# Performance work log

Hardware: AMD Instinct MI355X
Metric: run time of the kernel (lower is better)

The kernel has to match this reference:

```python
import jax, jax.numpy as jnp
import numpy as np

N = 100000      # nodes
E = 1000000     # edges per directional view
D = 128         # feature dim (all layers)
NG, OG = 4, 32  # n_gram_len, one_gram_dim (NG*OG == D)
L = 2           # conv layers (layer_dims=[128,128,128])
DEC = 64        # decoder hidden = D // 2
CLS = 64        # task classes
L2_EPS = 1e-12


def setup_inputs() -> dict:
    key = jax.random.key(0)
    ks = iter(jax.random.split(key, 40))
    nrm = lambda shape, s=0.05: jax.random.normal(next(ks), shape, dtype=jnp.float32) * s
    inp = {
        'x': jax.random.normal(next(ks), (N, D), dtype=jnp.float32),
        'edge_index_in': jax.random.randint(next(ks), (2, E), 0, N, dtype=jnp.int32),
        'edge_weight_in': jax.random.uniform(next(ks), (E,), dtype=jnp.float32),
        'edge_index_out': jax.random.randint(next(ks), (2, E), 0, N, dtype=jnp.int32),
        'edge_weight_out': jax.random.uniform(next(ks), (E,), dtype=jnp.float32),
        'edge_index_und': jax.random.randint(next(ks), (2, E), 0, N, dtype=jnp.int32),
        'edge_weight_und': jax.random.uniform(next(ks), (E,), dtype=jnp.float32),
        'pe': nrm((NG, OG)),
        # per-layer stacked params (both layers are D->D)
        'W_main_in': nrm((L, D, D)),
        'W_main_out': nrm((L, D, D)),
        'W_shared': nrm((L, D, D)),
        'W_und': nrm((L, D, D)),
        'b_main_in': nrm((L, D), 0.01),
        'b_main_out': nrm((L, D), 0.01),
        'b_shared_in': nrm((L, D), 0.01),
        'b_shared_out': nrm((L, D), 0.01),
        'b_und': nrm((L, D), 0.01),
        'C_in_vec': jnp.ones((L, N, 1), jnp.float32) + nrm((L, N, 1), 0.01),
        'C_out_vec': jnp.ones((L, N, 1), jnp.float32) + nrm((L, N, 1), 0.01),
        'C_all_vec': jnp.ones((L, N, 1), jnp.float32) + nrm((L, N, 1), 0.01),
        'constant': nrm((L, N, D)),
        'Wd1': nrm((DEC, D)),
        'bd1': nrm((DEC,), 0.01),
        'Wd2': nrm((CLS, DEC)),
        'bd2': nrm((CLS,), 0.01),
    }
    return inp


def reference(x, edge_index_in, edge_weight_in, edge_index_out, edge_weight_out,
              edge_index_und, edge_weight_und, pe,
              W_main_in, W_main_out, W_shared, W_und,
              b_main_in, b_main_out, b_shared_in, b_shared_out, b_und,
              C_in_vec, C_out_vec, C_all_vec, constant,
              Wd1, bd1, Wd2, bd2):
    n = x.shape[0]

    def prop(ei, ew, h):
        # message: edge_weight * x_j (gather from src=ei[0]); aggr='add' at dst=ei[1]
        msg = ew[:, None] * h[ei[0]]                      # [E, D]
        return jax.ops.segment_sum(msg, ei[1], num_segments=n)

    # positional encoding over n-gram sub-blocks
    h = (x.reshape(n, NG, OG) + pe[None]).reshape(n, NG * OG)

    for i in range(L):
        h_res = h
        hs = h @ W_shared[i].T                            # shared transform (computed once)
        ic = (prop(edge_index_in, edge_weight_in, h @ W_main_in[i].T) + b_main_in[i]
              + prop(edge_index_in, edge_weight_in, hs) + b_shared_in[i])
        oc = (prop(edge_index_out, edge_weight_out, h @ W_main_out[i].T) + b_main_out[i]
              + prop(edge_index_out, edge_weight_out, hs) + b_shared_out[i])
        ac = prop(edge_index_und, edge_weight_und, h @ W_und[i].T) + b_und[i]
        gcn = C_all_vec[i] * ac + C_in_vec[i] * ic + C_out_vec[i] * oc + constant[i]
        # res_proj is Identity (in_dim == out_dim); dropout inactive (eval)
        h = jax.nn.leaky_relu(gcn + h_res)

    z = jax.nn.relu(h @ Wd1.T + bd1)
    logits = z @ Wd2.T + bd2
    logp = jax.nn.log_softmax(logits, axis=-1)
    emb = h / jnp.maximum(jnp.linalg.norm(h, axis=-1, keepdims=True), L2_EPS)
    return (logp, emb)
```

## Files before the change

kernel.cpp:

```cpp
#include <hip/hip_runtime.h>
#include <math.h>

#define NN 100000
#define EE 1000000
#define DD 128
#define CLS 64

#define NB 196
#define CHUNK 4096
#define NCH 245
#define SLOTS (3 * NB * NCH)
#define CAPB 8192

typedef short bf16x8 __attribute__((ext_vector_type(8)));
typedef float f32x4 __attribute__((ext_vector_type(4)));

static __device__ __forceinline__ short f2bf(float f) {
  union { float f; unsigned u; } v; v.f = f;
  unsigned r = v.u + 0x7FFF + ((v.u >> 16) & 1);
  return (short)(r >> 16);
}
static __device__ __forceinline__ unsigned pack2(float a, float b) {
  return ((unsigned)(unsigned short)f2bf(b) << 16) | (unsigned short)f2bf(a);
}
static __device__ __forceinline__ float bf_lo(unsigned u) {
  union { unsigned u; float f; } v; v.u = u << 16; return v.f;
}
static __device__ __forceinline__ float bf_hi(unsigned u) {
  union { unsigned u; float f; } v; v.u = u & 0xffff0000u; return v.f;
}

__global__ __launch_bounds__(256) void pe_kernel(const float* __restrict__ x,
                                                 const float* __restrict__ pe,
                                                 short* __restrict__ h) {
  int idx8 = blockIdx.x * 256 + threadIdx.x;
  int d0 = (idx8 & 15) * 8;
  float4 a = *(const float4*)&x[(size_t)idx8 * 8];
  float4 b = *(const float4*)&x[(size_t)idx8 * 8 + 4];
  float4 pa = *(const float4*)&pe[d0];
  float4 pb = *(const float4*)&pe[d0 + 4];
  int4 o;
  o.x = pack2(a.x + pa.x, a.y + pa.y);
  o.y = pack2(a.z + pa.z, a.w + pa.w);
  o.z = pack2(b.x + pb.x, b.y + pb.y);
  o.w = pack2(b.z + pb.z, b.w + pb.w);
  *(int4*)&h[(size_t)idx8 * 8] = o;
}

__global__ __launch_bounds__(256) void wprep_kernel(const float* __restrict__ Wmi,
                                                    const float* __restrict__ Wmo,
                                                    const float* __restrict__ Wsh,
                                                    const float* __restrict__ Wu,
                                                    short* __restrict__ Wcat) {
  int idx = blockIdx.x * 256 + threadIdx.x;
  int l = idx / 49152;
  int r = idx - l * 49152;
  int j = r >> 7, k = r & 127;
  float v;
  if (j < 128)      v = Wmi[l*16384 + j*128 + k] + Wsh[l*16384 + j*128 + k];
  else if (j < 256) v = Wmo[l*16384 + (j-128)*128 + k] + Wsh[l*16384 + (j-128)*128 + k];
  else              v = Wu[l*16384 + (j-256)*128 + k];
  Wcat[idx] = f2bf(v);
}

__global__ __launch_bounds__(256) void countA_kernel(const int* __restrict__ ei0,
                                                     const int* __restrict__ ei1,
                                                     const int* __restrict__ ei2,
                                                     int* __restrict__ counts) {
  __shared__ int c[NB];
  int v = blockIdx.y, ch = blockIdx.x, tid = threadIdx.x;
  const int* dstp = ((v == 0) ? ei0 : (v == 1) ? ei1 : ei2) + EE;
  for (int i = tid; i < NB; i += 256) c[i] = 0;
  __syncthreads();
  int s = ch * CHUNK, e = (s + CHUNK < EE) ? s + CHUNK : EE;
  for (int i = s + tid; i < e; i += 256) atomicAdd(&c[dstp[i] >> 9], 1);
  __syncthreads();
  for (int b = tid; b < NB; b += 256) counts[(v * NB + b) * NCH + ch] = c[b];
}

__global__ __launch_bounds__(256) void scan1_kernel(const int* __restrict__ counts,
                                                    int* __restrict__ S,
                                                    int* __restrict__ bsums, int n) {
  __shared__ int sd[256];
  int t = threadIdx.x;
  int base = blockIdx.x * 1024 + t * 4;
  int4 v = make_int4(0, 0, 0, 0);
  if (base + 3 < n) {
    v = *(const int4*)&counts[base];
  } else {
    if (base + 0 < n) v.x = counts[base + 0];
    if (base + 1 < n) v.y = counts[base + 1];
    if (base + 2 < n) v.z = counts[base + 2];
    if (base + 3 < n) v.w = counts[base + 3];
  }
  int ts = v.x + v.y + v.z + v.w;
  sd[t] = ts;
  __syncthreads();
  for (int off = 1; off < 256; off <<= 1) {
    int xel = (t >= off) ? sd[t - off] : 0;
    __syncthreads();
    sd[t] += xel;
    __syncthreads();
  }
  int excl = sd[t] - ts;
  int o0 = excl, o1 = o0 + v.x, o2 = o1 + v.y, o3 = o2 + v.z;
  if (base + 0 < n) S[base + 0] = o0;
  if (base + 1 < n) S[base + 1] = o1;
  if (base + 2 < n) S[base + 2] = o2;
  if (base + 3 < n) S[base + 3] = o3;
  if (t == 255) bsums[blockIdx.x] = sd[255];
}

__global__ void scan2_kernel(int* __restrict__ bsums, int nb) {
  __shared__ int sd[512];
  int t = threadIdx.x;
  int v = (t < nb) ? bsums[t] : 0;
  sd[t] = v;
  __syncthreads();
  for (int off = 1; off < 512; off <<= 1) {
    int xel = (t >= off) ? sd[t - off] : 0;
    __syncthreads();
    sd[t] += xel;
    __syncthreads();
  }
  if (t < nb) bsums[t] = sd[t] - v;
}

__global__ __launch_bounds__(256) void scan3_kernel(int* __restrict__ S,
                                                    const int* __restrict__ bsums, int n) {
  int i = blockIdx.x * 256 + threadIdx.x;
  if (i < n) S[i] += bsums[i >> 10];
}

__global__ __launch_bounds__(256) void partA_kernel(const int* __restrict__ ei0,
                                                    const int* __restrict__ ei1,
                                                    const int* __restrict__ ei2,
                                                    const float* __restrict__ ew0,
                                                    const float* __restrict__ ew1,
                                                    const float* __restrict__ ew2,
                                                    const int* __restrict__ S,
                                                    int2* __restrict__ binned) {
  __shared__ int cur[NB];
  int v = blockIdx.y, ch = blockIdx.x, tid = threadIdx.x;
  const int* ei = (v == 0) ? ei0 : (v == 1) ? ei1 : ei2;
  const float* ew = (v == 0) ? ew0 : (v == 1) ? ew1 : ew2;
  for (int b = tid; b < NB; b += 256) cur[b] = S[(v * NB + b) * NCH + ch];
  __syncthreads();
  int s = ch * CHUNK, e = (s + CHUNK < EE) ? s + CHUNK : EE;
  for (int i = s + tid; i < e; i += 256) {
    int src = ei[i];
    int dst = ei[EE + i];
    float w = ew[i];
    int b = dst >> 9;
    int pos = atomicAdd(&cur[b], 1);
    binned[pos] = make_int2(src | ((dst & 511) << 17), __float_as_int(w));
  }
}

__global__ __launch_bounds__(256) void buildB_kernel(const int2* __restrict__ binned,
                                                     const int* __restrict__ S,
                                                     unsigned* __restrict__ csr4,
                                                     int* __restrict__ offs) {
  __shared__ int2 recs[CAPB];
  __shared__ int cnt[512];
  __shared__ int pref[512];
  __shared__ int sd[256];
  int gb = blockIdx.x, tid = threadIdx.x;
  int v = gb / NB, b = gb - v * NB;
  int base = S[gb * NCH];
  int next = (gb == 3 * NB - 1) ? 3 * EE : S[(gb + 1) * NCH];
  int n = next - base;
  for (int i = tid; i < 512; i += 256) cnt[i] = 0;
  int m = n < CAPB ? n : CAPB;
  for (int i = tid; i < m; i += 256) recs[i] = binned[base + i];
  __syncthreads();
  for (int i = tid; i < n; i += 256) {
    int2 r = (i < CAPB) ? recs[i] : binned[base + i];
    atomicAdd(&cnt[(r.x >> 17) & 511], 1);
  }
  __syncthreads();
  int c0 = cnt[2 * tid], c1 = cnt[2 * tid + 1];
  int ssum = c0 + c1;
  sd[tid] = ssum;
  __syncthreads();
  for (int off = 1; off < 256; off <<= 1) {
    int x = (tid >= off) ? sd[tid - off] : 0;
    __syncthreads();
    sd[tid] += x;
    __syncthreads();
  }
  int excl = sd[tid] - ssum;
  pref[2 * tid] = excl;
  pref[2 * tid + 1] = excl + c0;
  __syncthreads();
  int node0 = b * 512;
  for (int i = tid; i < 512; i += 256) {
    int node = node0 + i;
    if (node < NN) offs[v * NN + node] = base + pref[i];
  }
  if (gb == 0 && tid == 0) offs[3 * NN] = 3 * EE;
  for (int i = tid; i < 512; i += 256) cnt[i] = pref[i];
  __syncthreads();
  for (int i = tid; i < n; i += 256) {
    int2 r = (i < CAPB) ? recs[i] : binned[base + i];
    int nl = (r.x >> 17) & 511;
    int p = atomicAdd(&cnt[nl], 1);
    float w = __int_as_float(r.y);
    unsigned wb = (unsigned)(unsigned short)f2bf(w);
    csr4[base + p] = (wb << 17) | (unsigned)(r.x & 0x1FFFF);
  }
}

#define LW 136
__global__ __launch_bounds__(256) void mm_mfma(const short* __restrict__ H,
                                               const short* __restrict__ WcatL,
                                               short* __restrict__ tAll) {
  __shared__ short As[128 * LW];
  __shared__ short Bs[128 * LW];
  int tid = threadIdx.x;
  int rowbase = blockIdx.x * 128;

  for (int idx = tid; idx < 2048; idx += 256) {
    int r = idx >> 4, c8 = (idx & 15) * 8;
    int gr = rowbase + r; if (gr >= NN) gr = NN - 1;
    *(int4*)&As[r * LW + c8] = *(const int4*)&H[(size_t)gr * 128 + c8];
  }

  int w = tid >> 6, lane = tid & 63;
  int wr = (w >> 1) * 64, wc = (w & 1) * 64;
  int lrow = lane & 15, quad = lane >> 4;

  for (int view = 0; view < 3; ++view) {
    __syncthreads();
    for (int idx = tid; idx < 2048; idx += 256) {
      int r = idx >> 4, c8 = (idx & 15) * 8;
      *(int4*)&Bs[r * LW + c8] = *(const int4*)&WcatL[(view * 128 + r) * 128 + c8];
    }
    __syncthreads();

    f32x4 acc[4][4];
#pragma unroll
    for (int mi = 0; mi < 4; ++mi)
#pragma unroll
      for (int ni = 0; ni < 4; ++ni) acc[mi][ni] = (f32x4){0.f, 0.f, 0.f, 0.f};

#pragma unroll
    for (int k0 = 0; k0 < 128; k0 += 32) {
      bf16x8 a[4], b[4];
#pragma unroll
      for (int mi = 0; mi < 4; ++mi)
        a[mi] = *(const bf16x8*)&As[(wr + mi * 16 + lrow) * LW + k0 + quad * 8];
#pragma unroll
      for (int ni = 0; ni < 4; ++ni)
        b[ni] = *(const bf16x8*)&Bs[(wc + ni * 16 + lrow) * LW + k0 + quad * 8];
#pragma unroll
      for (int mi = 0; mi < 4; ++mi)
#pragma unroll
        for (int ni = 0; ni < 4; ++ni)
          acc[mi][ni] = __builtin_amdgcn_mfma_f32_16x16x32_bf16(a[mi], b[ni], acc[mi][ni], 0, 0, 0);
    }

    short* out = tAll + (size_t)view * ((size_t)NN * 128);
#pragma unroll
    for (int mi = 0; mi < 4; ++mi) {
#pragma unroll
      for (int ni = 0; ni < 4; ++ni) {
#pragma unroll
        for (int r = 0; r < 4; ++r) {
          int row = rowbase + wr + mi * 16 + quad * 4 + r;
          if (row < NN) {
            int col = wc + ni * 16 + lrow;
            out[(size_t)row * 128 + col] = f2bf(acc[mi][ni][r]);
          }
        }
      }
    }
  }
}

__global__ __launch_bounds__(256) void agg_kernel(
    const short* __restrict__ tAll, const unsigned* __restrict__ csr4,
    const int* __restrict__ offs, const short* __restrict__ h_prev,
    const float* __restrict__ b_mi, const float* __restrict__ b_mo,
    const float* __restrict__ b_si, const float* __restrict__ b_so,
    const float* __restrict__ b_u, const float* __restrict__ Cin,
    const float* __restrict__ Cout, const float* __restrict__ Call,
    const float* __restrict__ cst, short* __restrict__ h_out) {
  int gid = blockIdx.x * 256 + threadIdx.x;
  int v = gid >> 6;
  int lane = gid & 63;
  int f0 = lane * 2;
  float ax[3], ay[3];

#pragma unroll
  for (int view = 0; view < 3; ++view) {
    const short* t = tAll + (size_t)view * ((size_t)NN * 128);
    int s = offs[view * NN + v];
    int e = offs[view * NN + v + 1];
    float accx = 0.f, accy = 0.f;
    for (int base = s; base < e; base += 64) {
      int cnt = e - base; if (cnt > 64) cnt = 64;
      int r = 0;
      if (lane < cnt) r = (int)csr4[base + lane];
      int j = 0;
      for (; j + 3 < cnt; j += 4) {
        unsigned r0 = (unsigned)__shfl(r, j);
        unsigned r1 = (unsigned)__shfl(r, j + 1);
        unsigned r2 = (unsigned)__shfl(r, j + 2);
        unsigned r3 = (unsigned)__shfl(r, j + 3);
        float w0 = __uint_as_float((r0 >> 17) << 16);
        float w1 = __uint_as_float((r1 >> 17) << 16);
        float w2 = __uint_as_float((r2 >> 17) << 16);
        float w3 = __uint_as_float((r3 >> 17) << 16);
        unsigned u0 = *(const unsigned*)&t[(size_t)(r0 & 0x1FFFF) * 128 + f0];
        unsigned u1 = *(const unsigned*)&t[(size_t)(r1 & 0x1FFFF) * 128 + f0];
        unsigned u2 = *(const unsigned*)&t[(size_t)(r2 & 0x1FFFF) * 128 + f0];
        unsigned u3 = *(const unsigned*)&t[(size_t)(r3 & 0x1FFFF) * 128 + f0];
        accx += w0 * bf_lo(u0) + w1 * bf_lo(u1) + w2 * bf_lo(u2) + w3 * bf_lo(u3);
        accy += w0 * bf_hi(u0) + w1 * bf_hi(u1) + w2 * bf_hi(u2) + w3 * bf_hi(u3);
      }
      for (; j < cnt; ++j) {
        unsigned r0 = (unsigned)__shfl(r, j);
        float w0 = __uint_as_float((r0 >> 17) << 16);
        unsigned u0 = *(const unsigned*)&t[(size_t)(r0 & 0x1FFFF) * 128 + f0];
        accx += w0 * bf_lo(u0);
        accy += w0 * bf_hi(u0);
      }
    }
    ax[view] = accx; ay[view] = accy;
  }

  float ci = Cin[v], co = Cout[v], ca = Call[v];
  float2 bi = *(const float2*)&b_mi[f0];
  float2 bsi2 = *(const float2*)&b_si[f0];
  float2 bo = *(const float2*)&b_mo[f0];
  float2 bso2 = *(const float2*)&b_so[f0];
  float2 bu = *(const float2*)&b_u[f0];
  float2 cs = *(const float2*)&cst[(size_t)v * 128 + f0];
  unsigned hp = *(const unsigned*)&h_prev[(size_t)v * 128 + f0];

  float gx = ca * (ax[2] + bu.x) + ci * (ax[0] + bi.x + bsi2.x) +
             co * (ax[1] + bo.x + bso2.x) + cs.x + bf_lo(hp);
  float gy = ca * (ay[2] + bu.y) + ci * (ay[0] + bi.y + bsi2.y) +
             co * (ay[1] + bo.y + bso2.y) + cs.y + bf_hi(hp);
  gx = gx > 0.f ? gx : 0.01f * gx;
  gy = gy > 0.f ? gy : 0.01f * gy;
  *(unsigned*)&h_out[(size_t)v * 128 + f0] = pack2(gx, gy);
}

__global__ __launch_bounds__(256) void dec_kernel(const short* __restrict__ h,
                                                  const float* __restrict__ Wd1,
                                                  const float* __restrict__ bd1,
                                                  const float* __restrict__ Wd2,
                                                  const float* __restrict__ bd2,
                                                  float* __restrict__ out_logp,
                                                  float* __restrict__ out_emb) {
  __shared__ float Hs[32 * 128];
  __shared__ float W1t[64 * 66];
  __shared__ float W2t[64 * 66];
  __shared__ float Zs[32 * 68];
  int tid = threadIdx.x;
  int base = blockIdx.x * 32;

  for (int idx = tid; idx < 2048; idx += 256) {
    unsigned u = *(const unsigned*)&h[(size_t)base * 128 + idx * 2];
    Hs[idx * 2] = bf_lo(u);
    Hs[idx * 2 + 1] = bf_hi(u);
  }
  for (int idx = tid; idx < 4096; idx += 256) {
    int c = idx >> 6, k = idx & 63;
    W2t[k * 66 + c] = Wd2[idx];
  }

  int j = tid & 63;
  int rg = tid >> 6;
  float zacc[8];
#pragma unroll
  for (int r = 0; r < 8; ++r) zacc[r] = 0.f;

  for (int kk = 0; kk < 128; kk += 64) {
    __syncthreads();
    for (int idx = tid; idx < 4096; idx += 256) {
      int jj = idx >> 6, k = idx & 63;
      W1t[k * 66 + jj] = Wd1[jj * 128 + kk + k];
    }
    __syncthreads();
    for (int k = 0; k < 64; ++k) {
      float w = W1t[k * 66 + j];
#pragma unroll
      for (int r = 0; r < 8; ++r) zacc[r] += Hs[(rg * 8 + r) * 128 + kk + k] * w;
    }
  }
  float b1 = bd1[j];
#pragma unroll
  for (int r = 0; r < 8; ++r) {
    float z = zacc[r] + b1;
    Zs[(rg * 8 + r) * 68 + j] = z > 0.f ? z : 0.f;
  }
  __syncthreads();

  float b2 = bd2[j];
  float lg[8];
#pragma unroll
  for (int i = 0; i < 8; ++i) lg[i] = b2;
  for (int k = 0; k < 64; ++k) {
    float w = W2t[k * 66 + j];
#pragma unroll
    for (int i = 0; i < 8; ++i) lg[i] += Zs[(rg + 4 * i) * 68 + k] * w;
  }

#pragma unroll
  for (int i = 0; i < 8; ++i) {
    float m = lg[i];
    for (int d = 1; d < 64; d <<= 1) m = fmaxf(m, __shfl_xor(m, d));
    float s = expf(lg[i] - m);
    for (int d = 1; d < 64; d <<= 1) s += __shfl_xor(s, d);
    float lp = lg[i] - m - logf(s);
    out_logp[(size_t)(base + rg + 4 * i) * 64 + j] = lp;
  }

#pragma unroll
  for (int i = 0; i < 8; ++i) {
    int r = rg + 4 * i;
    float v1 = Hs[r * 128 + j];
    float v2 = Hs[r * 128 + 64 + j];
    float ss = v1 * v1 + v2 * v2;
    for (int d = 1; d < 64; d <<= 1) ss += __shfl_xor(ss, d);
    float nrm = sqrtf(ss);
    float sc = 1.f / fmaxf(nrm, 1e-12f);
    size_t o = (size_t)(base + r) * 128;
    out_emb[o + j] = v1 * sc;
    out_emb[o + 64 + j] = v2 * sc;
  }
}

extern "C" void kernel_launch(void* const* d_in, const int* in_sizes, int n_in,
                              void* d_out, int out_size, void* d_ws, size_t ws_size,
                              hipStream_t stream) {
  const float* x   = (const float*)d_in[0];
  const int* eiI   = (const int*)d_in[1];
  const float* ewI = (const float*)d_in[2];
  const int* eiO   = (const int*)d_in[3];
  const float* ewO = (const float*)d_in[4];
  const int* eiU   = (const int*)d_in[5];
  const float* ewU = (const float*)d_in[6];
  const float* pe  = (const float*)d_in[7];
  const float* Wmi = (const float*)d_in[8];
  const float* Wmo = (const float*)d_in[9];
  const float* Wsh = (const float*)d_in[10];
  const float* Wu  = (const float*)d_in[11];
  const float* bmi = (const float*)d_in[12];
  const float* bmo = (const float*)d_in[13];
  const float* bsi = (const float*)d_in[14];
  const float* bso = (const float*)d_in[15];
  const float* bu  = (const float*)d_in[16];
  const float* Cin = (const float*)d_in[17];
  const float* Cou = (const float*)d_in[18];
  const float* Cal = (const float*)d_in[19];
  const float* cst = (const float*)d_in[20];
  const float* Wd1 = (const float*)d_in[21];
  const float* bd1 = (const float*)d_in[22];
  const float* Wd2 = (const float*)d_in[23];
  const float* bd2 = (const float*)d_in[24];

  const size_t ND = (size_t)NN * DD;
  short* wsS = (short*)d_ws;
  short* hA   = wsS;
  short* hB   = hA + ND;
  short* tAll = hB + ND;
  short* Wcat = tAll + 3 * ND;
  int2* binned   = (int2*)(Wcat + 98304);
  unsigned* csr4 = (unsigned*)(binned + (size_t)3 * EE);
  int* S      = (int*)(csr4 + (size_t)3 * EE);
  int* bsums  = S + SLOTS + 4;
  int* offs   = bsums + 512;

  pe_kernel<<<6250, 256, 0, stream>>>(x, pe, hA);
  wprep_kernel<<<384, 256, 0, stream>>>(Wmi, Wmo, Wsh, Wu, Wcat);

  dim3 chGrid(NCH, 3);
  countA_kernel<<<chGrid, 256, 0, stream>>>(eiI, eiO, eiU, S);
  const int nb1 = (SLOTS + 1023) / 1024;
  scan1_kernel<<<nb1, 256, 0, stream>>>(S, S, bsums, SLOTS);
  scan2_kernel<<<1, 512, 0, stream>>>(bsums, nb1);
  scan3_kernel<<<(SLOTS + 255) / 256, 256, 0, stream>>>(S, bsums, SLOTS);
  partA_kernel<<<chGrid, 256, 0, stream>>>(eiI, eiO, eiU, ewI, ewO, ewU, S, binned);
  buildB_kernel<<<3 * NB, 256, 0, stream>>>(binned, S, csr4, offs);

  const short* hin = hA;
  short* hout = hB;
  dim3 mmGrid((NN + 127) / 128);
  for (int l = 0; l < 2; ++l) {
    mm_mfma<<<mmGrid, 256, 0, stream>>>(hin, Wcat + l * 49152, tAll);
    agg_kernel<<<25000, 256, 0, stream>>>(tAll, csr4, offs, hin,
                                          bmi + l * DD, bmo + l * DD, bsi + l * DD,
                                          bso + l * DD, bu + l * DD, Cin + l * NN,
                                          Cou + l * NN, Cal + l * NN,
                                          cst + (size_t)l * NN * DD, hout);
    short* tmp = (short*)hin;
    hin = hout;
    hout = tmp;
  }

  float* out_logp = (float*)d_out;
  float* out_emb = out_logp + (size_t)NN * CLS;
  dec_kernel<<<3125, 256, 0, stream>>>(hin, Wd1, bd1, Wd2, bd2, out_logp, out_emb);
}
```

Measured before the change: 790.2 us.

## Stage GEMM output through LDS for vector stores; split aggregation wave into edge halves

The transform GEMM epilogue now writes its bf16 results into shared memory and then stores whole rows to global memory with 16-byte vector writes, instead of scattered 2-byte stores. The aggregation kernel splits each 64-lane wave into two half-waves that each process alternate edges with 8-byte feature loads (4 features per lane). The two halves' partial sums are combined with a cross-lane xor shuffle. This aims to cut store transactions and raise gather width and memory-level parallelism, at the cost of extra syncs, LDS reuse of the B tile, and a final shuffle reduction.

```diff
diff --git a/kernel.cpp b/kernel.cpp
--- a/kernel.cpp
+++ b/kernel.cpp
@@ -260,20 +260,25 @@
           acc[mi][ni] = __builtin_amdgcn_mfma_f32_16x16x32_bf16(a[mi], b[ni], acc[mi][ni], 0, 0, 0);
     }
 
+    __syncthreads();
+#pragma unroll
+    for (int mi = 0; mi < 4; ++mi)
+#pragma unroll
+      for (int ni = 0; ni < 4; ++ni)
+#pragma unroll
+        for (int r = 0; r < 4; ++r) {
+          int rl = wr + mi * 16 + quad * 4 + r;
+          int cl = wc + ni * 16 + lrow;
+          Bs[rl * LW + cl] = f2bf(acc[mi][ni][r]);
+        }
+    __syncthreads();
+
     short* out = tAll + (size_t)view * ((size_t)NN * 128);
-#pragma unroll
-    for (int mi = 0; mi < 4; ++mi) {
-#pragma unroll
-      for (int ni = 0; ni < 4; ++ni) {
-#pragma unroll
-        for (int r = 0; r < 4; ++r) {
-          int row = rowbase + wr + mi * 16 + quad * 4 + r;
-          if (row < NN) {
-            int col = wc + ni * 16 + lrow;
-            out[(size_t)row * 128 + col] = f2bf(acc[mi][ni][r]);
-          }
-        }
-      }
+    for (int idx = tid; idx < 2048; idx += 256) {
+      int r = idx >> 4, c8 = (idx & 15) * 8;
+      int row = rowbase + r;
+      if (row < NN)
+        *(int4*)&out[(size_t)row * 128 + c8] = *(const int4*)&Bs[r * LW + c8];
     }
   }
 }
@@ -289,63 +294,94 @@
   int gid = blockIdx.x * 256 + threadIdx.x;
   int v = gid >> 6;
   int lane = gid & 63;
-  int f0 = lane * 2;
-  float ax[3], ay[3];
+  int m = lane & 31;
+  int hh = lane >> 5;
+  int f0 = m * 4;
+  float a[3][4];
 
 #pragma unroll
   for (int view = 0; view < 3; ++view) {
     const short* t = tAll + (size_t)view * ((size_t)NN * 128);
     int s = offs[view * NN + v];
     int e = offs[view * NN + v + 1];
-    float accx = 0.f, accy = 0.f;
-    for (int base = s; base < e; base += 64) {
-      int cnt = e - base; if (cnt > 64) cnt = 64;
-      int r = 0;
-      if (lane < cnt) r = (int)csr4[base + lane];
-      int j = 0;
-      for (; j + 3 < cnt; j += 4) {
-        unsigned r0 = (unsigned)__shfl(r, j);
-        unsigned r1 = (unsigned)__shfl(r, j + 1);
-        unsigned r2 = (unsigned)__shfl(r, j + 2);
-        unsigned r3 = (unsigned)__shfl(r, j + 3);
-        float w0 = __uint_as_float((r0 >> 17) << 16);
-        float w1 = __uint_as_float((r1 >> 17) << 16);
-        float w2 = __uint_as_float((r2 >> 17) << 16);
-        float w3 = __uint_as_float((r3 >> 17) << 16);
-        unsigned u0 = *(const unsigned*)&t[(size_t)(r0 & 0x1FFFF) * 128 + f0];
-        unsigned u1 = *(const unsigned*)&t[(size_t)(r1 & 0x1FFFF) * 128 + f0];
-        unsigned u2 = *(const unsigned*)&t[(size_t)(r2 & 0x1FFFF) * 128 + f0];
-        unsigned u3 = *(const unsigned*)&t[(size_t)(r3 & 0x1FFFF) * 128 + f0];
-        accx += w0 * bf_lo(u0) + w1 * bf_lo(u1) + w2 * bf_lo(u2) + w3 * bf_lo(u3);
-        accy += w0 * bf_hi(u0) + w1 * bf_hi(u1) + w2 * bf_hi(u2) + w3 * bf_hi(u3);
+    int cnt = e - s;
+    int npair = cnt >> 1;
+    float a0 = 0.f, a1 = 0.f, a2 = 0.f, a3 = 0.f;
+    int i = 0;
+    for (; i + 1 < npair; i += 2) {
+      unsigned q0 = csr4[s + 2 * i + 0];
+      unsigned q1 = csr4[s + 2 * i + 1];
+      unsigned q2 = csr4[s + 2 * i + 2];
+      unsigned q3 = csr4[s + 2 * i + 3];
+      unsigned rA = hh ? q1 : q0;
+      unsigned rB = hh ? q3 : q2;
+      float wA = __uint_as_float((rA >> 17) << 16);
+      float wB = __uint_as_float((rB >> 17) << 16);
+      uint2 uA = *(const uint2*)&t[(size_t)(rA & 0x1FFFF) * 128 + f0];
+      uint2 uB = *(const uint2*)&t[(size_t)(rB & 0x1FFFF) * 128 + f0];
+      a0 += wA * bf_lo(uA.x) + wB * bf_lo(uB.x);
+      a1 += wA * bf_hi(uA.x) + wB * bf_hi(uB.x);
+      a2 += wA * bf_lo(uA.y) + wB * bf_lo(uB.y);
+      a3 += wA * bf_hi(uA.y) + wB * bf_hi(uB.y);
+    }
+    for (; i < npair; ++i) {
+      unsigned q0 = csr4[s + 2 * i + 0];
+      unsigned q1 = csr4[s + 2 * i + 1];
+      unsigned rA = hh ? q1 : q0;
+      float wA = __uint_as_float((rA >> 17) << 16);
+      uint2 uA = *(const uint2*)&t[(size_t)(rA & 0x1FFFF) * 128 + f0];
+      a0 += wA * bf_lo(uA.x);
+      a1 += wA * bf_hi(uA.x);
+      a2 += wA * bf_lo(uA.y);
+      a3 += wA * bf_hi(uA.y);
+    }
+    if (cnt & 1) {
+      unsigned r0 = csr4[e - 1];
+      float w0 = __uint_as_float((r0 >> 17) << 16);
+      uint2 u0 = *(const uint2*)&t[(size_t)(r0 & 0x1FFFF) * 128 + f0];
+      if (hh == 0) {
+        a0 += w0 * bf_lo(u0.x);
+        a1 += w0 * bf_hi(u0.x);
+        a2 += w0 * bf_lo(u0.y);
+        a3 += w0 * bf_hi(u0.y);
       }
-      for (; j < cnt; ++j) {
-        unsigned r0 = (unsigned)__shfl(r, j);
-        float w0 = __uint_as_float((r0 >> 17) << 16);
-        unsigned u0 = *(const unsigned*)&t[(size_t)(r0 & 0x1FFFF) * 128 + f0];
-        accx += w0 * bf_lo(u0);
-        accy += w0 * bf_hi(u0);
-      }
-    }
-    ax[view] = accx; ay[view] = accy;
-  }
+    }
+    a[view][0] = a0; a[view][1] = a1; a[view][2] = a2; a[view][3] = a3;
+  }
+
+#pragma unroll
+  for (int view = 0; view < 3; ++view)
+#pragma unroll
+    for (int k = 0; k < 4; ++k)
+      a[view][k] += __shfl_xor(a[view][k], 32);
 
   float ci = Cin[v], co = Cout[v], ca = Call[v];
-  float2 bi = *(const float2*)&b_mi[f0];
-  float2 bsi2 = *(const float2*)&b_si[f0];
-  float2 bo = *(const float2*)&b_mo[f0];
-  float2 bso2 = *(const float2*)&b_so[f0];
-  float2 bu = *(const float2*)&b_u[f0];
-  float2 cs = *(const float2*)&cst[(size_t)v * 128 + f0];
-  unsigned hp = *(const unsigned*)&h_prev[(size_t)v * 128 + f0];
-
-  float gx = ca * (ax[2] + bu.x) + ci * (ax[0] + bi.x + bsi2.x) +
-             co * (ax[1] + bo.x + bso2.x) + cs.x + bf_lo(hp);
-  float gy = ca * (ay[2] + bu.y) + ci * (ay[0] + bi.y + bsi2.y) +
-             co * (ay[1] + bo.y + bso2.y) + cs.y + bf_hi(hp);
-  gx = gx > 0.f ? gx : 0.01f * gx;
-  gy = gy > 0.f ? gy : 0.01f * gy;
-  *(unsigned*)&h_out[(size_t)v * 128 + f0] = pack2(gx, gy);
+  float4 bi = *(const float4*)&b_mi[f0];
+  float4 bsi4 = *(const float4*)&b_si[f0];
+  float4 bo = *(const float4*)&b_mo[f0];
+  float4 bso4 = *(const float4*)&b_so[f0];
+  float4 bu = *(const float4*)&b_u[f0];
+  float4 cs = *(const float4*)&cst[(size_t)v * 128 + f0];
+  uint2 hp = *(const uint2*)&h_prev[(size_t)v * 128 + f0];
+
+  float g0 = ca * (a[2][0] + bu.x) + ci * (a[0][0] + bi.x + bsi4.x) +
+             co * (a[1][0] + bo.x + bso4.x) + cs.x + bf_lo(hp.x);
+  float g1 = ca * (a[2][1] + bu.y) + ci * (a[0][1] + bi.y + bsi4.y) +
+             co * (a[1][1] + bo.y + bso4.y) + cs.y + bf_hi(hp.x);
+  float g2 = ca * (a[2][2] + bu.z) + ci * (a[0][2] + bi.z + bsi4.z) +
+             co * (a[1][2] + bo.z + bso4.z) + cs.z + bf_lo(hp.y);
+  float g3 = ca * (a[2][3] + bu.w) + ci * (a[0][3] + bi.w + bsi4.w) +
+             co * (a[1][3] + bo.w + bso4.w) + cs.w + bf_hi(hp.y);
+  g0 = g0 > 0.f ? g0 : 0.01f * g0;
+  g1 = g1 > 0.f ? g1 : 0.01f * g1;
+  g2 = g2 > 0.f ? g2 : 0.01f * g2;
+  g3 = g3 > 0.f ? g3 : 0.01f * g3;
+  if (hh == 0) {
+    uint2 o;
+    o.x = pack2(g0, g1);
+    o.y = pack2(g2, g3);
+    *(uint2*)&h_out[(size_t)v * 128 + f0] = o;
+  }
 }
 
 __global__ __launch_bounds__(256) void dec_kernel(const short* __restrict__ h,
```

Measured after the change: 829.3 us. 4.9% more time.

## Aggregate raw features before transform and fuse combine into GEMM epilogue

Applied to the files above, without the earlier changes.

Reorders each layer so the sparse aggregation runs on h directly (A·h) for all three views, and a single GEMM kernel then scales each view's aggregate by its per-node C coefficient and accumulates all three transforms into one accumulator. Bias, constant, residual and leaky ReLU move into the GEMM epilogue, which is staged through shared memory for coalesced stores. This keeps the gather traffic the same but removes the separate per-view GEMM outputs and the combine pass. The cost is an extra bf16 rounding of the aggregates and of the C-scaled values before the MFMA, which changes precision.

```diff
diff --git a/kernel.cpp b/kernel.cpp
--- a/kernel.cpp
+++ b/kernel.cpp
@@ -28,6 +28,9 @@
 }
 static __device__ __forceinline__ float bf_hi(unsigned u) {
   union { unsigned u; float f; } v; v.u = u & 0xffff0000u; return v.f;
+}
+static __device__ __forceinline__ float bfs(short s) {
+  union { unsigned u; float f; } v; v.u = ((unsigned)(unsigned short)s) << 16; return v.f;
 }
 
 __global__ __launch_bounds__(256) void pe_kernel(const float* __restrict__ x,
@@ -211,90 +214,16 @@
   }
 }
 
-#define LW 136
-__global__ __launch_bounds__(256) void mm_mfma(const short* __restrict__ H,
-                                               const short* __restrict__ WcatL,
-                                               short* __restrict__ tAll) {
-  __shared__ short As[128 * LW];
-  __shared__ short Bs[128 * LW];
-  int tid = threadIdx.x;
-  int rowbase = blockIdx.x * 128;
-
-  for (int idx = tid; idx < 2048; idx += 256) {
-    int r = idx >> 4, c8 = (idx & 15) * 8;
-    int gr = rowbase + r; if (gr >= NN) gr = NN - 1;
-    *(int4*)&As[r * LW + c8] = *(const int4*)&H[(size_t)gr * 128 + c8];
-  }
-
-  int w = tid >> 6, lane = tid & 63;
-  int wr = (w >> 1) * 64, wc = (w & 1) * 64;
-  int lrow = lane & 15, quad = lane >> 4;
-
-  for (int view = 0; view < 3; ++view) {
-    __syncthreads();
-    for (int idx = tid; idx < 2048; idx += 256) {
-      int r = idx >> 4, c8 = (idx & 15) * 8;
-      *(int4*)&Bs[r * LW + c8] = *(const int4*)&WcatL[(view * 128 + r) * 128 + c8];
-    }
-    __syncthreads();
-
-    f32x4 acc[4][4];
-#pragma unroll
-    for (int mi = 0; mi < 4; ++mi)
-#pragma unroll
-      for (int ni = 0; ni < 4; ++ni) acc[mi][ni] = (f32x4){0.f, 0.f, 0.f, 0.f};
-
-#pragma unroll
-    for (int k0 = 0; k0 < 128; k0 += 32) {
-      bf16x8 a[4], b[4];
-#pragma unroll
-      for (int mi = 0; mi < 4; ++mi)
-        a[mi] = *(const bf16x8*)&As[(wr + mi * 16 + lrow) * LW + k0 + quad * 8];
-#pragma unroll
-      for (int ni = 0; ni < 4; ++ni)
-        b[ni] = *(const bf16x8*)&Bs[(wc + ni * 16 + lrow) * LW + k0 + quad * 8];
-#pragma unroll
-      for (int mi = 0; mi < 4; ++mi)
-#pragma unroll
-        for (int ni = 0; ni < 4; ++ni)
-          acc[mi][ni] = __builtin_amdgcn_mfma_f32_16x16x32_bf16(a[mi], b[ni], acc[mi][ni], 0, 0, 0);
-    }
-
-    short* out = tAll + (size_t)view * ((size_t)NN * 128);
-#pragma unroll
-    for (int mi = 0; mi < 4; ++mi) {
-#pragma unroll
-      for (int ni = 0; ni < 4; ++ni) {
-#pragma unroll
-        for (int r = 0; r < 4; ++r) {
-          int row = rowbase + wr + mi * 16 + quad * 4 + r;
-          if (row < NN) {
-            int col = wc + ni * 16 + lrow;
-            out[(size_t)row * 128 + col] = f2bf(acc[mi][ni][r]);
-          }
-        }
-      }
-    }
-  }
-}
-
-__global__ __launch_bounds__(256) void agg_kernel(
-    const short* __restrict__ tAll, const unsigned* __restrict__ csr4,
-    const int* __restrict__ offs, const short* __restrict__ h_prev,
-    const float* __restrict__ b_mi, const float* __restrict__ b_mo,
-    const float* __restrict__ b_si, const float* __restrict__ b_so,
-    const float* __restrict__ b_u, const float* __restrict__ Cin,
-    const float* __restrict__ Cout, const float* __restrict__ Call,
-    const float* __restrict__ cst, short* __restrict__ h_out) {
+__global__ __launch_bounds__(256) void agg3_kernel(
+    const short* __restrict__ h, const unsigned* __restrict__ csr4,
+    const int* __restrict__ offs, short* __restrict__ g) {
   int gid = blockIdx.x * 256 + threadIdx.x;
   int v = gid >> 6;
   int lane = gid & 63;
   int f0 = lane * 2;
-  float ax[3], ay[3];
 
 #pragma unroll
   for (int view = 0; view < 3; ++view) {
-    const short* t = tAll + (size_t)view * ((size_t)NN * 128);
     int s = offs[view * NN + v];
     int e = offs[view * NN + v + 1];
     float accx = 0.f, accy = 0.f;
@@ -312,40 +241,130 @@
         float w1 = __uint_as_float((r1 >> 17) << 16);
         float w2 = __uint_as_float((r2 >> 17) << 16);
         float w3 = __uint_as_float((r3 >> 17) << 16);
-        unsigned u0 = *(const unsigned*)&t[(size_t)(r0 & 0x1FFFF) * 128 + f0];
-        unsigned u1 = *(const unsigned*)&t[(size_t)(r1 & 0x1FFFF) * 128 + f0];
-        unsigned u2 = *(const unsigned*)&t[(size_t)(r2 & 0x1FFFF) * 128 + f0];
-        unsigned u3 = *(const unsigned*)&t[(size_t)(r3 & 0x1FFFF) * 128 + f0];
+        unsigned u0 = *(const unsigned*)&h[(size_t)(r0 & 0x1FFFF) * 128 + f0];
+        unsigned u1 = *(const unsigned*)&h[(size_t)(r1 & 0x1FFFF) * 128 + f0];
+        unsigned u2 = *(const unsigned*)&h[(size_t)(r2 & 0x1FFFF) * 128 + f0];
+        unsigned u3 = *(const unsigned*)&h[(size_t)(r3 & 0x1FFFF) * 128 + f0];
         accx += w0 * bf_lo(u0) + w1 * bf_lo(u1) + w2 * bf_lo(u2) + w3 * bf_lo(u3);
         accy += w0 * bf_hi(u0) + w1 * bf_hi(u1) + w2 * bf_hi(u2) + w3 * bf_hi(u3);
       }
       for (; j < cnt; ++j) {
         unsigned r0 = (unsigned)__shfl(r, j);
         float w0 = __uint_as_float((r0 >> 17) << 16);
-        unsigned u0 = *(const unsigned*)&t[(size_t)(r0 & 0x1FFFF) * 128 + f0];
+        unsigned u0 = *(const unsigned*)&h[(size_t)(r0 & 0x1FFFF) * 128 + f0];
         accx += w0 * bf_lo(u0);
         accy += w0 * bf_hi(u0);
       }
     }
-    ax[view] = accx; ay[view] = accy;
-  }
-
-  float ci = Cin[v], co = Cout[v], ca = Call[v];
-  float2 bi = *(const float2*)&b_mi[f0];
-  float2 bsi2 = *(const float2*)&b_si[f0];
-  float2 bo = *(const float2*)&b_mo[f0];
-  float2 bso2 = *(const float2*)&b_so[f0];
-  float2 bu = *(const float2*)&b_u[f0];
-  float2 cs = *(const float2*)&cst[(size_t)v * 128 + f0];
-  unsigned hp = *(const unsigned*)&h_prev[(size_t)v * 128 + f0];
-
-  float gx = ca * (ax[2] + bu.x) + ci * (ax[0] + bi.x + bsi2.x) +
-             co * (ax[1] + bo.x + bso2.x) + cs.x + bf_lo(hp);
-  float gy = ca * (ay[2] + bu.y) + ci * (ay[0] + bi.y + bsi2.y) +
-             co * (ay[1] + bo.y + bso2.y) + cs.y + bf_hi(hp);
-  gx = gx > 0.f ? gx : 0.01f * gx;
-  gy = gy > 0.f ? gy : 0.01f * gy;
-  *(unsigned*)&h_out[(size_t)v * 128 + f0] = pack2(gx, gy);
+    *(unsigned*)&g[(size_t)view * ((size_t)NN * 128) + (size_t)v * 128 + f0] =
+        pack2(accx, accy);
+  }
+}
+
+#define LW 136
+__global__ __launch_bounds__(256) void mmc_kernel(
+    const short* __restrict__ g, const short* __restrict__ WcatL,
+    const float* __restrict__ b_mi, const float* __restrict__ b_mo,
+    const float* __restrict__ b_si, const float* __restrict__ b_so,
+    const float* __restrict__ b_u,
+    const float* __restrict__ Cin, const float* __restrict__ Cou,
+    const float* __restrict__ Cal,
+    const float* __restrict__ cst, const short* __restrict__ h_prev,
+    short* __restrict__ h_out) {
+  __shared__ short As[128 * LW];
+  __shared__ short Bs[128 * LW];
+  __shared__ float cvs[3][128];
+  __shared__ float bias[3][128];
+  int tid = threadIdx.x;
+  int rowbase = blockIdx.x * 128;
+
+  if (tid < 128) {
+    int r = tid;
+    int gr = rowbase + r; if (gr >= NN) gr = NN - 1;
+    cvs[0][r] = Cin[gr];
+    cvs[1][r] = Cou[gr];
+    cvs[2][r] = Cal[gr];
+  } else {
+    int c = tid - 128;
+    bias[0][c] = b_mi[c] + b_si[c];
+    bias[1][c] = b_mo[c] + b_so[c];
+    bias[2][c] = b_u[c];
+  }
+
+  int w = tid >> 6, lane = tid & 63;
+  int wr = (w >> 1) * 64, wc = (w & 1) * 64;
+  int lrow = lane & 15, quad = lane >> 4;
+
+  f32x4 comb[4][4];
+#pragma unroll
+  for (int mi = 0; mi < 4; ++mi)
+#pragma unroll
+    for (int ni = 0; ni < 4; ++ni) comb[mi][ni] = (f32x4){0.f, 0.f, 0.f, 0.f};
+
+  for (int view = 0; view < 3; ++view) {
+    __syncthreads();
+    const short* gv = g + (size_t)view * ((size_t)NN * 128);
+    for (int idx = tid; idx < 2048; idx += 256) {
+      int r = idx >> 4, c8 = (idx & 15) * 8;
+      int gr = rowbase + r; if (gr >= NN) gr = NN - 1;
+      float cv = cvs[view][r];
+      int4 u = *(const int4*)&gv[(size_t)gr * 128 + c8];
+      int4 o;
+      o.x = pack2(cv * bf_lo((unsigned)u.x), cv * bf_hi((unsigned)u.x));
+      o.y = pack2(cv * bf_lo((unsigned)u.y), cv * bf_hi((unsigned)u.y));
+      o.z = pack2(cv * bf_lo((unsigned)u.z), cv * bf_hi((unsigned)u.z));
+      o.w = pack2(cv * bf_lo((unsigned)u.w), cv * bf_hi((unsigned)u.w));
+      *(int4*)&As[r * LW + c8] = o;
+      *(int4*)&Bs[r * LW + c8] = *(const int4*)&WcatL[(view * 128 + r) * 128 + c8];
+    }
+    __syncthreads();
+
+#pragma unroll
+    for (int k0 = 0; k0 < 128; k0 += 32) {
+      bf16x8 a[4], b[4];
+#pragma unroll
+      for (int mi = 0; mi < 4; ++mi)
+        a[mi] = *(const bf16x8*)&As[(wr + mi * 16 + lrow) * LW + k0 + quad * 8];
+#pragma unroll
+      for (int ni = 0; ni < 4; ++ni)
+        b[ni] = *(const bf16x8*)&Bs[(wc + ni * 16 + lrow) * LW + k0 + quad * 8];
+#pragma unroll
+      for (int mi = 0; mi < 4; ++mi)
+#pragma unroll
+        for (int ni = 0; ni < 4; ++ni)
+          comb[mi][ni] = __builtin_amdgcn_mfma_f32_16x16x32_bf16(a[mi], b[ni], comb[mi][ni], 0, 0, 0);
+    }
+  }
+
+  __syncthreads();
+#pragma unroll
+  for (int mi = 0; mi < 4; ++mi) {
+#pragma unroll
+    for (int r = 0; r < 4; ++r) {
+      int rl = wr + mi * 16 + quad * 4 + r;
+      int row = rowbase + rl;
+      int grow = (row < NN) ? row : NN - 1;
+      float ci = cvs[0][rl], co = cvs[1][rl], ca = cvs[2][rl];
+#pragma unroll
+      for (int ni = 0; ni < 4; ++ni) {
+        int cl = wc + ni * 16 + lrow;
+        float val = comb[mi][ni][r]
+                  + ci * bias[0][cl] + co * bias[1][cl] + ca * bias[2][cl]
+                  + cst[(size_t)grow * 128 + cl]
+                  + bfs(h_prev[(size_t)grow * 128 + cl]);
+        val = val > 0.f ? val : 0.01f * val;
+        Bs[rl * LW + cl] = f2bf(val);
+      }
+    }
+  }
+  __syncthreads();
+
+  for (int idx = tid; idx < 2048; idx += 256) {
+    int r = idx >> 4, c8 = (idx & 15) * 8;
+    int row = rowbase + r;
+    if (row < NN)
+      *(int4*)&h_out[(size_t)row * 128 + c8] = *(const int4*)&Bs[r * LW + c8];
+  }
 }
 
 __global__ __launch_bounds__(256) void dec_kernel(const short* __restrict__ h,
@@ -467,8 +486,8 @@
   short* wsS = (short*)d_ws;
   short* hA   = wsS;
   short* hB   = hA + ND;
-  short* tAll = hB + ND;
-  short* Wcat = tAll + 3 * ND;
+  short* g    = hB + ND;
+  short* Wcat = g + 3 * ND;
   int2* binned   = (int2*)(Wcat + 98304);
   unsigned* csr4 = (unsigned*)(binned + (size_t)3 * EE);
   int* S      = (int*)(csr4 + (size_t)3 * EE);
@@ -491,12 +510,12 @@
   short* hout = hB;
   dim3 mmGrid((NN + 127) / 128);
   for (int l = 0; l < 2; ++l) {
-    mm_mfma<<<mmGrid, 256, 0, stream>>>(hin, Wcat + l * 49152, tAll);
-    agg_kernel<<<25000, 256, 0, stream>>>(tAll, csr4, offs, hin,
-                                          bmi + l * DD, bmo + l * DD, bsi + l * DD,
-                                          bso + l * DD, bu + l * DD, Cin + l * NN,
-                                          Cou + l * NN, Cal + l * NN,
-                                          cst + (size_t)l * NN * DD, hout);
+    agg3_kernel<<<25000, 256, 0, stream>>>(hin, csr4, offs, g);
+    mmc_kernel<<<mmGrid, 256, 0, stream>>>(g, Wcat + l * 49152,
+                                           bmi + l * DD, bmo + l * DD,
+                                           bsi + l * DD, bso + l * DD, bu + l * DD,
+                                           Cin + l * NN, Cou + l * NN, Cal + l * NN,
+                                           cst + (size_t)l * ND, hin, hout);
     short* tmp = (short*)hin;
     hin = hout;
     hout = tmp;
```

Result: slower. 821.0 us (+3.9%).
